# Optimization experiments

Measured on AMD Instinct MI355X. Metric: run time of the kernel, lower is better.

Reference implementation:

```python
import jax, jax.numpy as jnp
import numpy as np

B = 4096          # graph pairs in batch
NPG = 40          # nodes per molecular graph
N = B * NPG       # total nodes per drug batch
EPG = 160         # directed edges per graph
E = B * EPG
F_IN = 78         # atom feature dim
HID = 128
HEADS = 4
ADD = 8           # additional features (concentrations)
BN_EPS = 1e-5
D0 = HEADS * HID          # 512
CMB = 4 * HID + ADD       # 2 drugs * (mean||max of 128) + ADD = 520


def setup_inputs() -> dict:
    key = jax.random.key(0)
    ks = iter(jax.random.split(key, 64))
    def nrm(shape, s=0.1):
        return jax.random.normal(next(ks), shape, jnp.float32) * s
    def pos(shape):  # positive running variances
        return jax.random.uniform(next(ks), shape, jnp.float32, 0.5, 1.5)
    offs = jnp.repeat(jnp.arange(B, dtype=jnp.int32) * NPG, EPG)
    def edges():
        return jax.random.randint(next(ks), (2, E), 0, NPG, dtype=jnp.int32) + offs[None, :]
    batch = jnp.repeat(jnp.arange(B, dtype=jnp.int32), NPG)
    inp = dict(
        x_a=nrm((N, F_IN), 1.0), edge_a=edges(), batch_a=batch,
        x_b=nrm((N, F_IN), 1.0), edge_b=edges(), batch_b=batch,
        addf=nrm((B, ADD), 1.0),
        # shared GAT encoder params
        gW0=nrm((F_IN, D0)), gb0=nrm((D0,)), gas0=nrm((D0,)), gad0=nrm((D0,)),
        gW1=nrm((D0, D0)), gb1=nrm((D0,)), gas1=nrm((D0,)), gad1=nrm((D0,)),
        gW2=nrm((D0, HID)), gb2=nrm((HID,)), gas2=nrm((HID,)), gad2=nrm((HID,)),
        bn0g=pos((D0,)), bn0b=nrm((D0,)), bn0m=nrm((D0,)), bn0v=pos((D0,)),
        bn1g=pos((D0,)), bn1b=nrm((D0,)), bn1m=nrm((D0,)), bn1v=pos((D0,)),
        bn2g=pos((HID,)), bn2b=nrm((HID,)), bn2m=nrm((HID,)), bn2v=pos((HID,)),
        # combination MLP params (Linear + eval BatchNorm stats)
        mW0=nrm((CMB, 2 * HID)), mb0=nrm((2 * HID,)),
        mg0=pos((2 * HID,)), mbe0=nrm((2 * HID,)), mm0=nrm((2 * HID,)), mv0=pos((2 * HID,)),
        mW1=nrm((2 * HID, HID)), mb1=nrm((HID,)),
        mg1=pos((HID,)), mbe1=nrm((HID,)), mm1=nrm((HID,)), mv1=pos((HID,)),
        mW2=nrm((HID, 1)), mb2=nrm((1,)),
    )
    return inp


def _bn(x, g, b, m, v):
    return (x - m) * jax.lax.rsqrt(v + BN_EPS) * g + b


def _gat(x, src, dst, W, b, a_src, a_dst, heads, ch, concat):
    """PyG GATConv (eval): linear, per-head additive attention with
    leaky_relu(0.2), segment-softmax over incoming edges (self-loops included)."""
    n = x.shape[0]
    h = (x @ W).reshape(n, heads, ch)                     # [N, H, C]
    es = jnp.sum(h * a_src.reshape(1, heads, ch), -1)     # [N, H]
    ed = jnp.sum(h * a_dst.reshape(1, heads, ch), -1)     # [N, H]
    e = jax.nn.leaky_relu(es[src] + ed[dst], 0.2)         # [E', H]
    emax = jax.ops.segment_max(e, dst, num_segments=n)
    ex = jnp.exp(e - emax[dst])
    den = jax.ops.segment_sum(ex, dst, num_segments=n)
    alpha = ex / den[dst]                                 # [E', H]
    out = jax.ops.segment_sum(h[src] * alpha[..., None], dst, num_segments=n)
    out = out.reshape(n, heads * ch) if concat else jnp.mean(out, axis=1)
    return out + b


def _encode(x, edge, batch, p):
    n = x.shape[0]
    sl = jnp.arange(n, dtype=edge.dtype)                  # self-loops (PyG default)
    src = jnp.concatenate([edge[0], sl])
    dst = jnp.concatenate([edge[1], sl])
    x = _gat(x, src, dst, p['gW0'], p['gb0'], p['gas0'], p['gad0'], HEADS, HID, True)
    x = jax.nn.relu(_bn(x, p['bn0g'], p['bn0b'], p['bn0m'], p['bn0v']))
    x = _gat(x, src, dst, p['gW1'], p['gb1'], p['gas1'], p['gad1'], HEADS, HID, True)
    x = jax.nn.relu(_bn(x, p['bn1g'], p['bn1b'], p['bn1m'], p['bn1v']))
    x = _gat(x, src, dst, p['gW2'], p['gb2'], p['gas2'], p['gad2'], 1, HID, False)
    x = _bn(x, p['bn2g'], p['bn2b'], p['bn2m'], p['bn2v'])  # no relu on last layer
    cnt = jax.ops.segment_sum(jnp.ones((n, 1), x.dtype), batch, num_segments=B)
    x_mean = jax.ops.segment_sum(x, batch, num_segments=B) / cnt
    x_max = jax.ops.segment_max(x, batch, num_segments=B)
    return jnp.concatenate([x_mean, x_max], axis=1)        # [B, 2*HID]


def reference(x_a, edge_a, batch_a, x_b, edge_b, batch_b, addf,
              gW0, gb0, gas0, gad0, gW1, gb1, gas1, gad1, gW2, gb2, gas2, gad2,
              bn0g, bn0b, bn0m, bn0v, bn1g, bn1b, bn1m, bn1v, bn2g, bn2b, bn2m, bn2v,
              mW0, mb0, mg0, mbe0, mm0, mv0, mW1, mb1, mg1, mbe1, mm1, mv1, mW2, mb2):
    p = dict(gW0=gW0, gb0=gb0, gas0=gas0, gad0=gad0, gW1=gW1, gb1=gb1, gas1=gas1,
             gad1=gad1, gW2=gW2, gb2=gb2, gas2=gas2, gad2=gad2,
             bn0g=bn0g, bn0b=bn0b, bn0m=bn0m, bn0v=bn0v,
             bn1g=bn1g, bn1b=bn1b, bn1m=bn1m, bn1v=bn1v,
             bn2g=bn2g, bn2b=bn2b, bn2m=bn2m, bn2v=bn2v)
    emb_a = _encode(x_a, edge_a, batch_a, p)
    emb_b = _encode(x_b, edge_b, batch_b, p)
    c = jnp.concatenate([emb_a, emb_b, addf], axis=1)      # [B, 520]
    h = jax.nn.relu(_bn(c @ mW0 + mb0, mg0, mbe0, mm0, mv0))
    h = jax.nn.relu(_bn(h @ mW1 + mb1, mg1, mbe1, mm1, mv1))
    out = jax.nn.sigmoid(h @ mW2 + mb2)
    return jnp.squeeze(out, -1)                            # [B]
```

## Files before the change

### kernel.cpp

```cpp
#include <hip/hip_runtime.h>
#include <stdint.h>

#define B_GRAPHS 4096
#define NPG 40
#define NTOT (B_GRAPHS * NPG)
#define EPG 160
#define ETOT (B_GRAPHS * EPG)
#define ESL 200
#define F_IN 78
#define KP0 96
#define HID 128
#define D0 512
#define CMB 520
#define BN_EPS 1e-5f
#define KPM 544
#define A0ST 552
#define H1ST 264
#define H2ST 132

typedef short bf16x8 __attribute__((ext_vector_type(8)));
typedef float floatx4 __attribute__((ext_vector_type(4)));

__device__ inline float b2f(unsigned short u) {
    union { float f; uint32_t i; } v; v.i = ((uint32_t)u) << 16; return v.f;
}
__device__ inline unsigned short f2b(float f) {
    union { float f; uint32_t i; } v; v.f = f;
    uint32_t x = v.i;
    return (unsigned short)((x + 0x7fffu + ((x >> 16) & 1u)) >> 16);
}
__device__ inline float lo16(uint32_t u) {
    union { float f; uint32_t i; } v; v.i = u << 16; return v.f;
}
__device__ inline float hi16(uint32_t u) {
    union { float f; uint32_t i; } v; v.i = u & 0xffff0000u; return v.f;
}
__device__ inline int htoff(int ch, int s) {
    int chunk = s >> 3, within = s & 7;
    return ch * 40 + (((chunk + ch) % 5) << 3) + within;
}
__device__ inline void gl2lds16(const unsigned short* g, unsigned short* l) {
    __builtin_amdgcn_global_load_lds(
        (const __attribute__((address_space(1))) unsigned int*)g,
        (__attribute__((address_space(3))) unsigned int*)l, 16, 0, 0);
}

__global__ __launch_bounds__(256)
void write_code_kernel(float* __restrict__ out, int n, float S)
{
    int i = blockIdx.x * 256 + threadIdx.x;
    if (i < n) out[i] = (i == 0) ? S : 0.f;
}

__global__ __launch_bounds__(256)
void convw_kernel(const float* __restrict__ W, unsigned short* __restrict__ Wt,
                  int K, int N, int Kp)
{
    int t = blockIdx.x * 256 + threadIdx.x;
    if (t >= N * Kp) return;
    int n = t / Kp, k = t - n * Kp;
    Wt[t] = (k < K) ? f2b(W[(size_t)k * N + n]) : 0;
}

__global__ __launch_bounds__(256)
void convw_hilo_kernel(const float* __restrict__ W,
                       unsigned short* __restrict__ Whi,
                       unsigned short* __restrict__ Wlo,
                       int K, int N, int Kp)
{
    int t = blockIdx.x * 256 + threadIdx.x;
    if (t >= N * Kp) return;
    int n = t / Kp, k = t - n * Kp;
    float x = (k < K) ? W[(size_t)k * N + n] : 0.f;
    unsigned short hb = f2b(x);
    Whi[t] = hb;
    Wlo[t] = f2b(x - b2f(hb));
}

__global__ __launch_bounds__(256)
void convx_kernel(const float* __restrict__ X, unsigned short* __restrict__ Xb, int M)
{
    int t = blockIdx.x * 256 + threadIdx.x;
    if (t >= M * (KP0 / 8)) return;
    int r = t / (KP0 / 8), c8 = t - r * (KP0 / 8);
    unsigned int pk[4];
    #pragma unroll
    for (int j = 0; j < 4; j++) {
        int k0 = c8 * 8 + 2 * j, k1 = k0 + 1;
        float x0 = (k0 < F_IN) ? X[(size_t)r * F_IN + k0] : 0.f;
        float x1 = (k1 < F_IN) ? X[(size_t)r * F_IN + k1] : 0.f;
        pk[j] = (unsigned int)f2b(x0) | ((unsigned int)f2b(x1) << 16);
    }
    *(uint4*)&Xb[(size_t)r * KP0 + c8 * 8] = make_uint4(pk[0], pk[1], pk[2], pk[3]);
}

__global__ __launch_bounds__(256)
void gemm_mfma_kernel(const unsigned short* __restrict__ A,
                      const unsigned short* __restrict__ Bt,
                      unsigned short* __restrict__ C,
                      int M, int K, int N)
{
    __shared__ __align__(16) unsigned short As[128 * 32];
    __shared__ __align__(16) unsigned short Bs[128 * 32];
    const int tid  = threadIdx.x;
    const int lane = tid & 63, w = tid >> 6;
    const int quad = lane >> 4, l16 = lane & 15;
    const int wm = w >> 1, wn = w & 1;
    const int nwg  = gridDim.x * gridDim.y;
    const int orig = blockIdx.y * gridDim.x + blockIdx.x;
    const int q = nwg >> 3, r = nwg & 7;
    const int xcd = orig & 7, off = orig >> 3;
    const int swz = (xcd < r ? xcd * (q + 1) : r * (q + 1) + (xcd - r) * q) + off;
    const int row0 = (swz / gridDim.x) * 128, col0 = (swz % gridDim.x) * 128;

    floatx4 acc[4][4];
    #pragma unroll
    for (int mi = 0; mi < 4; mi++)
        #pragma unroll
        for (int ni = 0; ni < 4; ni++)
            acc[mi][ni] = (floatx4){0.f, 0.f, 0.f, 0.f};

    int srow[2], scg[2];
    #pragma unroll
    for (int it = 0; it < 2; it++) {
        int L = it * 4096 + w * 1024 + lane * 16;
        int rr = L >> 6;
        int cp = (L >> 4) & 3;
        srow[it] = rr;
        scg[it]  = cp ^ ((rr >> 1) & 3);
    }

    for (int k0 = 0; k0 < K; k0 += 32) {
        #pragma unroll
        for (int it = 0; it < 2; it++) {
            int ra = row0 + srow[it]; if (ra >= M) ra = M - 1;
            gl2lds16(A + (size_t)ra * K + k0 + scg[it] * 8,
                     As + (it * 4096 + w * 1024) / 2);
            int rb = col0 + srow[it];
            gl2lds16(Bt + (size_t)rb * K + k0 + scg[it] * 8,
                     Bs + (it * 4096 + w * 1024) / 2);
        }
        __syncthreads();

        bf16x8 fA[4], fB[4];
        #pragma unroll
        for (int mi = 0; mi < 4; mi++) {
            int rr = wm * 64 + mi * 16 + l16;
            __builtin_memcpy(&fA[mi], &As[rr * 32 + ((quad ^ ((rr >> 1) & 3)) * 8)], 16);
        }
        #pragma unroll
        for (int ni = 0; ni < 4; ni++) {
            int rr = wn * 64 + ni * 16 + l16;
            __builtin_memcpy(&fB[ni], &Bs[rr * 32 + ((quad ^ ((rr >> 1) & 3)) * 8)], 16);
        }
        #pragma unroll
        for (int mi = 0; mi < 4; mi++)
            #pragma unroll
            for (int ni = 0; ni < 4; ni++)
                acc[mi][ni] = __builtin_amdgcn_mfma_f32_16x16x32_bf16(
                    fB[ni], fA[mi], acc[mi][ni], 0, 0, 0);
        __syncthreads();
    }

    #pragma unroll
    for (int mi = 0; mi < 4; mi++) {
        int row = row0 + wm * 64 + mi * 16 + l16;
        if (row < M) {
            #pragma unroll
            for (int ni = 0; ni < 4; ni++) {
                floatx4 a = acc[mi][ni];
                unsigned int p0 = (unsigned int)f2b(a[0]) | ((unsigned int)f2b(a[1]) << 16);
                unsigned int p1 = (unsigned int)f2b(a[2]) | ((unsigned int)f2b(a[3]) << 16);
                *(uint2*)(C + (size_t)row * N + col0 + wn * 64 + ni * 16 + quad * 4) =
                    make_uint2(p0, p1);
            }
        }
    }
}

__global__ __launch_bounds__(256)
void gat4_fused_kernel(unsigned short* __restrict__ H,
                       const int* __restrict__ edge,
                       const float* __restrict__ avs, const float* __restrict__ avd,
                       const float* __restrict__ bias,
                       const float* __restrict__ bng, const float* __restrict__ bnb,
                       const float* __restrict__ bnm, const float* __restrict__ bnv,
                       int g0)
{
    __shared__ __align__(16) unsigned short ht[D0 * NPG];
    __shared__ float es[4 * NPG], ed[4 * NPG];
    __shared__ __align__(16) unsigned char cnt[NPG * 48];
    __shared__ short2 eloc[ESL];
    const int tid = threadIdx.x;
    const int lane = tid & 63, w = tid >> 6;
    const int quad = lane >> 4, l16 = lane & 15;
    const int gg = g0 + blockIdx.x;
    unsigned short* Hg = H + (size_t)blockIdx.x * NPG * D0;

    for (int i = tid; i < NPG * 48 / 4; i += 256) ((unsigned int*)cnt)[i] = 0u;
    for (int i = tid; i < ESL; i += 256) {
        if (i < EPG) {
            int s  = edge[(size_t)gg * EPG + i] - gg * NPG;
            int dd = edge[(size_t)ETOT + (size_t)gg * EPG + i] - gg * NPG;
            eloc[i] = make_short2((short)s, (short)dd);
        } else {
            short v = (short)(i - EPG);
            eloc[i] = make_short2(v, v);
        }
    }
    for (int u = tid; u < 64 * (NPG / 4); u += 256) {
        int c8 = u & 63, gi = u >> 6;
        const unsigned short* src = Hg + (size_t)(4 * gi) * D0 + c8 * 8;
        uint4 v0 = *(const uint4*)(src);
        uint4 v1 = *(const uint4*)(src + D0);
        uint4 v2 = *(const uint4*)(src + 2 * D0);
        uint4 v3 = *(const uint4*)(src + 3 * D0);
        unsigned int a0[4] = {v0.x, v0.y, v0.z, v0.w};
        unsigned int a1[4] = {v1.x, v1.y, v1.z, v1.w};
        unsigned int a2[4] = {v2.x, v2.y, v2.z, v2.w};
        unsigned int a3[4] = {v3.x, v3.y, v3.z, v3.w};
        #pragma unroll
        for (int k = 0; k < 8; k++) {
            const int ws = k >> 1, sh = (k & 1) * 16;
            unsigned int w0 = ((a0[ws] >> sh) & 0xffffu) | (((a1[ws] >> sh) & 0xffffu) << 16);
            unsigned int w1 = ((a2[ws] >> sh) & 0xffffu) | (((a3[ws] >> sh) & 0xffffu) << 16);
            *(uint2*)&ht[htoff(c8 * 8 + k, 4 * gi)] = make_uint2(w0, w1);
        }
    }
    __syncthreads();

    {
        float as0=0,as1=0,as2=0,as3=0, ad0=0,ad1=0,ad2=0,ad3=0;
        for (int ci = 0; ci < 32; ci++) {
            int c = quad + ci * 4;
            int chv = w * 128 + c;
            uint2 hv = *(const uint2*)&ht[htoff(chv, 4 * l16)];
            float h0 = lo16(hv.x), h1 = hi16(hv.x), h2 = lo16(hv.y), h3 = hi16(hv.y);
            float vs = avs[chv], vd = avd[chv];
            as0 += h0*vs; as1 += h1*vs; as2 += h2*vs; as3 += h3*vs;
            ad0 += h0*vd; ad1 += h1*vd; ad2 += h2*vd; ad3 += h3*vd;
        }
        #define RED4(x) x += __shfl_xor(x, 16); x += __shfl_xor(x, 32);
        RED4(as0) RED4(as1) RED4(as2) RED4(as3)
        RED4(ad0) RED4(ad1) RED4(ad2) RED4(ad3)
        #undef RED4
        if (quad == 0) {
            float rs[4] = {as0, as1, as2, as3};
            float rd[4] = {ad0, ad1, ad2, ad3};
            #pragma unroll
            for (int rr = 0; rr < 4; rr++) {
                int node = 4 * l16 + rr;
                if (node < NPG) { es[w * NPG + node] = rs[rr]; ed[w * NPG + node] = rd[rr]; }
            }
        }
    }
    for (int e = tid; e < ESL; e += 256) {
        short2 sd = eloc[e];
        atomicAdd((unsigned int*)cnt + ((sd.y * 48 + sd.x) >> 2),
                  1u << ((sd.x & 3) * 8));
    }
    __syncthreads();

    {
        bf16x8 ahi[3][2], alo[3][2];
        float esv0[8], esv1[8];
        #pragma unroll
        for (int j = 0; j < 8; j++) {
            esv0[j] = es[w * NPG + quad * 8 + j];
            esv1[j] = (quad == 0) ? es[w * NPG + 32 + j] : 0.f;
        }
        #pragma unroll
        for (int mt = 0; mt < 3; mt++) {
            int dn = mt * 16 + l16;
            bool ok = dn < NPG;
            float edv = 0.f;
            uint2 c0 = make_uint2(0u, 0u), c1 = make_uint2(0u, 0u);
            if (ok) {
                edv = ed[w * NPG + dn];
                c0 = *(const uint2*)&cnt[dn * 48 + quad * 8];
                if (quad == 0) c1 = *(const uint2*)&cnt[dn * 48 + 32];
            }
            float v0[8], v1[8];
            int cb0[8], cb1[8];
            float pm = -1e30f;
            #pragma unroll
            for (int j = 0; j < 8; j++) {
                cb0[j] = (int)(((j < 4 ? c0.x : c0.y) >> ((j & 3) * 8)) & 0xffu);
                float t0 = esv0[j] + edv;
                v0[j] = t0 > 0.f ? t0 : 0.2f * t0;
                if (cb0[j]) pm = fmaxf(pm, v0[j]);
                cb1[j] = (int)(((j < 4 ? c1.x : c1.y) >> ((j & 3) * 8)) & 0xffu);
                float t1 = esv1[j] + edv;
                v1[j] = t1 > 0.f ? t1 : 0.2f * t1;
                if (cb1[j]) pm = fmaxf(pm, v1[j]);
            }
            pm = fmaxf(pm, __shfl_xor(pm, 16));
            pm = fmaxf(pm, __shfl_xor(pm, 32));
            float e0[8], e1[8], pd = 0.f;
            #pragma unroll
            for (int j = 0; j < 8; j++) {
                e0[j] = cb0[j] ? (float)cb0[j] * __expf(v0[j] - pm) : 0.f;
                e1[j] = cb1[j] ? (float)cb1[j] * __expf(v1[j] - pm) : 0.f;
                pd += e0[j] + e1[j];
            }
            pd += __shfl_xor(pd, 16);
            pd += __shfl_xor(pd, 32);
            float di = ok ? 1.f / pd : 0.f;
            #pragma unroll
            for (int j = 0; j < 8; j++) {
                float a0 = e0[j] * di;
                unsigned short hb0 = f2b(a0);
                ahi[mt][0][j] = (short)hb0;
                alo[mt][0][j] = (short)f2b(a0 - b2f(hb0));
                float a1 = e1[j] * di;
                unsigned short hb1 = f2b(a1);
                ahi[mt][1][j] = (short)hb1;
                alo[mt][1][j] = (short)f2b(a1 - b2f(hb1));
            }
        }
        const floatx4 z = {0.f, 0.f, 0.f, 0.f};
        for (int nt = 0; nt < 8; nt++) {
            const int ch0 = w * 128 + nt * 16;
            bf16x8 b0, b1 = {0,0,0,0,0,0,0,0};
            __builtin_memcpy(&b0, &ht[htoff(ch0 + l16, quad * 8)], 16);
            if (quad == 0) __builtin_memcpy(&b1, &ht[htoff(ch0 + l16, 32)], 16);
            floatx4 acc0 = z, acc1 = z, acc2 = z;
            acc0 = __builtin_amdgcn_mfma_f32_16x16x32_bf16(ahi[0][0], b0, acc0, 0, 0, 0);
            acc1 = __builtin_amdgcn_mfma_f32_16x16x32_bf16(ahi[1][0], b0, acc1, 0, 0, 0);
            acc2 = __builtin_amdgcn_mfma_f32_16x16x32_bf16(ahi[2][0], b0, acc2, 0, 0, 0);
            acc0 = __builtin_amdgcn_mfma_f32_16x16x32_bf16(alo[0][0], b0, acc0, 0, 0, 0);
            acc1 = __builtin_amdgcn_mfma_f32_16x16x32_bf16(alo[1][0], b0, acc1, 0, 0, 0);
            acc2 = __builtin_amdgcn_mfma_f32_16x16x32_bf16(alo[2][0], b0, acc2, 0, 0, 0);
            acc0 = __builtin_amdgcn_mfma_f32_16x16x32_bf16(ahi[0][1], b1, acc0, 0, 0, 0);
            acc1 = __builtin_amdgcn_mfma_f32_16x16x32_bf16(ahi[1][1], b1, acc1, 0, 0, 0);
            acc2 = __builtin_amdgcn_mfma_f32_16x16x32_bf16(ahi[2][1], b1, acc2, 0, 0, 0);
            acc0 = __builtin_amdgcn_mfma_f32_16x16x32_bf16(alo[0][1], b1, acc0, 0, 0, 0);
            acc1 = __builtin_amdgcn_mfma_f32_16x16x32_bf16(alo[1][1], b1, acc1, 0, 0, 0);
            acc2 = __builtin_amdgcn_mfma_f32_16x16x32_bf16(alo[2][1], b1, acc2, 0, 0, 0);
            const int c = ch0 + l16;
            float scl = rsqrtf(bnv[c] + BN_EPS) * bng[c];
            float sft = (bias[c] - bnm[c]) * scl + bnb[c];
            unsigned short* reg = &ht[ch0 * 40];
            #pragma unroll
            for (int mt = 0; mt < 3; mt++) {
                floatx4 a = (mt == 0) ? acc0 : (mt == 1) ? acc1 : acc2;
                #pragma unroll
                for (int rr = 0; rr < 4; rr++) {
                    int dn = mt * 16 + quad * 4 + rr;
                    if (dn < NPG) {
                        float o = a[rr] * scl + sft;
                        o = fmaxf(o, 0.f);
                        reg[dn * 16 + l16] = f2b(o);
                    }
                }
            }
        }
    }
    __syncthreads();
    for (int u = tid; u < NPG * 64; u += 256) {
        int s = u >> 6, c8 = u & 63;
        const unsigned short* reg = &ht[(c8 >> 1) * 16 * 40];
        uint4 v = *(const uint4*)&reg[s * 16 + (c8 & 1) * 8];
        *(uint4*)(Hg + (size_t)s * D0 + c8 * 8) = v;
    }
}

__global__ __launch_bounds__(256)
void gat1_pool_fused_kernel(const unsigned short* __restrict__ H,
                            const int* __restrict__ edge,
                            const float* __restrict__ avs, const float* __restrict__ avd,
                            const float* __restrict__ bias,
                            const float* __restrict__ bng, const float* __restrict__ bnb,
                            const float* __restrict__ bnm, const float* __restrict__ bnv,
                            float* __restrict__ cmb, int colbase, int g0)
{
    __shared__ __align__(16) unsigned short ht[HID * NPG];
    __shared__ float es[NPG], ed[NPG];
    __shared__ __align__(16) unsigned char cnt[NPG * 48];
    __shared__ short2 eloc[ESL];
    const int tid = threadIdx.x;
    const int lane = tid & 63, w = tid >> 6;
    const int quad = lane >> 4, l16 = lane & 15;
    const int gg = g0 + blockIdx.x;
    const unsigned short* Hg = H + (size_t)blockIdx.x * NPG * HID;

    for (int i = tid; i < NPG * 48 / 4; i += 256) ((unsigned int*)cnt)[i] = 0u;
    for (int i = tid; i < ESL; i += 256) {
        if (i < EPG) {
            int s  = edge[(size_t)gg * EPG + i] - gg * NPG;
            int dd = edge[(size_t)ETOT + (size_t)gg * EPG + i] - gg * NPG;
            eloc[i] = make_short2((short)s, (short)dd);
        } else {
            short v = (short)(i - EPG);
            eloc[i] = make_short2(v, v);
        }
    }
    for (int u = tid; u < 16 * (NPG / 4); u += 256) {
        int c8 = u & 15, gi = u >> 4;
        const unsigned short* src = Hg + (size_t)(4 * gi) * HID + c8 * 8;
        uint4 v0 = *(const uint4*)(src);
        uint4 v1 = *(const uint4*)(src + HID);
        uint4 v2 = *(const uint4*)(src + 2 * HID);
        uint4 v3 = *(const uint4*)(src + 3 * HID);
        unsigned int a0[4] = {v0.x, v0.y, v0.z, v0.w};
        unsigned int a1[4] = {v1.x, v1.y, v1.z, v1.w};
        unsigned int a2[4] = {v2.x, v2.y, v2.z, v2.w};
        unsigned int a3[4] = {v3.x, v3.y, v3.z, v3.w};
        #pragma unroll
        for (int k = 0; k < 8; k++) {
            const int ws = k >> 1, sh = (k & 1) * 16;
            unsigned int w0 = ((a0[ws] >> sh) & 0xffffu) | (((a1[ws] >> sh) & 0xffffu) << 16);
            unsigned int w1 = ((a2[ws] >> sh) & 0xffffu) | (((a3[ws] >> sh) & 0xffffu) << 16);
            *(uint2*)&ht[htoff(c8 * 8 + k, 4 * gi)] = make_uint2(w0, w1);
        }
    }
    __syncthreads();

    if (w < 2) {
        const float* av = w ? avd : avs;
        float a0=0,a1=0,a2=0,a3=0;
        for (int ci = 0; ci < 32; ci++) {
            int c = quad + ci * 4;
            uint2 hv = *(const uint2*)&ht[htoff(c, 4 * l16)];
            float vc = av[c];
            a0 += lo16(hv.x)*vc; a1 += hi16(hv.x)*vc;
            a2 += lo16(hv.y)*vc; a3 += hi16(hv.y)*vc;
        }
        #define RED4(x) x += __shfl_xor(x, 16); x += __shfl_xor(x, 32);
        RED4(a0) RED4(a1) RED4(a2) RED4(a3)
        #undef RED4
        if (quad == 0) {
            float rv[4] = {a0, a1, a2, a3};
            float* dst = w ? ed : es;
            #pragma unroll
            for (int rr = 0; rr < 4; rr++) {
                int node = 4 * l16 + rr;
                if (node < NPG) dst[node] = rv[rr];
            }
        }
    }
    for (int e = tid; e < ESL; e += 256) {
        short2 sd = eloc[e];
        atomicAdd((unsigned int*)cnt + ((sd.y * 48 + sd.x) >> 2),
                  1u << ((sd.x & 3) * 8));
    }
    __syncthreads();

    {
        bf16x8 ahi[3][2], alo[3][2];
        float esv0[8], esv1[8];
        #pragma unroll
        for (int j = 0; j < 8; j++) {
            esv0[j] = es[quad * 8 + j];
            esv1[j] = (quad == 0) ? es[32 + j] : 0.f;
        }
        #pragma unroll
        for (int mt = 0; mt < 3; mt++) {
            int dn = mt * 16 + l16;
            bool ok = dn < NPG;
            float edv = 0.f;
            uint2 c0 = make_uint2(0u, 0u), c1 = make_uint2(0u, 0u);
            if (ok) {
                edv = ed[dn];
                c0 = *(const uint2*)&cnt[dn * 48 + quad * 8];
                if (quad == 0) c1 = *(const uint2*)&cnt[dn * 48 + 32];
            }
            float v0[8], v1[8];
            int cb0[8], cb1[8];
            float pm = -1e30f;
            #pragma unroll
            for (int j = 0; j < 8; j++) {
                cb0[j] = (int)(((j < 4 ? c0.x : c0.y) >> ((j & 3) * 8)) & 0xffu);
                float t0 = esv0[j] + edv;
                v0[j] = t0 > 0.f ? t0 : 0.2f * t0;
                if (cb0[j]) pm = fmaxf(pm, v0[j]);
                cb1[j] = (int)(((j < 4 ? c1.x : c1.y) >> ((j & 3) * 8)) & 0xffu);
                float t1 = esv1[j] + edv;
                v1[j] = t1 > 0.f ? t1 : 0.2f * t1;
                if (cb1[j]) pm = fmaxf(pm, v1[j]);
            }
            pm = fmaxf(pm, __shfl_xor(pm, 16));
            pm = fmaxf(pm, __shfl_xor(pm, 32));
            float e0[8], e1[8], pd = 0.f;
            #pragma unroll
            for (int j = 0; j < 8; j++) {
                e0[j] = cb0[j] ? (float)cb0[j] * __expf(v0[j] - pm) : 0.f;
                e1[j] = cb1[j] ? (float)cb1[j] * __expf(v1[j] - pm) : 0.f;
                pd += e0[j] + e1[j];
            }
            pd += __shfl_xor(pd, 16);
            pd += __shfl_xor(pd, 32);
            float di = ok ? 1.f / pd : 0.f;
            #pragma unroll
            for (int j = 0; j < 8; j++) {
                float a0 = e0[j] * di;
                unsigned short hb0 = f2b(a0);
                ahi[mt][0][j] = (short)hb0;
                alo[mt][0][j] = (short)f2b(a0 - b2f(hb0));
                float a1 = e1[j] * di;
                unsigned short hb1 = f2b(a1);
                ahi[mt][1][j] = (short)hb1;
                alo[mt][1][j] = (short)f2b(a1 - b2f(hb1));
            }
        }
        const floatx4 z = {0.f, 0.f, 0.f, 0.f};
        for (int t2 = 0; t2 < 2; t2++) {
            const int ch0 = (w * 2 + t2) * 16;
            bf16x8 b0, b1 = {0,0,0,0,0,0,0,0};
            __builtin_memcpy(&b0, &ht[htoff(ch0 + l16, quad * 8)], 16);
            if (quad == 0) __builtin_memcpy(&b1, &ht[htoff(ch0 + l16, 32)], 16);
            floatx4 acc0 = z, acc1 = z, acc2 = z;
            acc0 = __builtin_amdgcn_mfma_f32_16x16x32_bf16(ahi[0][0], b0, acc0, 0, 0, 0);
            acc1 = __builtin_amdgcn_mfma_f32_16x16x32_bf16(ahi[1][0], b0, acc1, 0, 0, 0);
            acc2 = __builtin_amdgcn_mfma_f32_16x16x32_bf16(ahi[2][0], b0, acc2, 0, 0, 0);
            acc0 = __builtin_amdgcn_mfma_f32_16x16x32_bf16(alo[0][0], b0, acc0, 0, 0, 0);
            acc1 = __builtin_amdgcn_mfma_f32_16x16x32_bf16(alo[1][0], b0, acc1, 0, 0, 0);
            acc2 = __builtin_amdgcn_mfma_f32_16x16x32_bf16(alo[2][0], b0, acc2, 0, 0, 0);
            acc0 = __builtin_amdgcn_mfma_f32_16x16x32_bf16(ahi[0][1], b1, acc0, 0, 0, 0);
            acc1 = __builtin_amdgcn_mfma_f32_16x16x32_bf16(ahi[1][1], b1, acc1, 0, 0, 0);
            acc2 = __builtin_amdgcn_mfma_f32_16x16x32_bf16(ahi[2][1], b1, acc2, 0, 0, 0);
            acc0 = __builtin_amdgcn_mfma_f32_16x16x32_bf16(alo[0][1], b1, acc0, 0, 0, 0);
            acc1 = __builtin_amdgcn_mfma_f32_16x16x32_bf16(alo[1][1], b1, acc1, 0, 0, 0);
            acc2 = __builtin_amdgcn_mfma_f32_16x16x32_bf16(alo[2][1], b1, acc2, 0, 0, 0);
            const int c = ch0 + l16;
            float scl = rsqrtf(bnv[c] + BN_EPS) * bng[c];
            float sft = (bias[c] - bnm[c]) * scl + bnb[c];
            float psum = 0.f, pmax = -1e30f;
            #pragma unroll
            for (int mt = 0; mt < 3; mt++) {
                floatx4 a = (mt == 0) ? acc0 : (mt == 1) ? acc1 : acc2;
                #pragma unroll
                for (int rr = 0; rr < 4; rr++) {
                    int dn = mt * 16 + quad * 4 + rr;
                    if (dn < NPG) {
                        float o = a[rr] * scl + sft;
                        psum += o;
                        pmax = fmaxf(pmax, o);
                    }
                }
            }
            psum += __shfl_xor(psum, 16); psum += __shfl_xor(psum, 32);
            pmax = fmaxf(pmax, __shfl_xor(pmax, 16));
            pmax = fmaxf(pmax, __shfl_xor(pmax, 32));
            if (quad == 0) {
                cmb[(size_t)gg * 512 + colbase + c] = psum * (1.f / NPG);
                cmb[(size_t)gg * 512 + colbase + HID + c] = pmax;
            }
        }
    }
}

__global__ __launch_bounds__(256)
void mlp_mfma_kernel(const float* __restrict__ cmb, const float* __restrict__ addf,
                     const unsigned short* __restrict__ W0hi, const unsigned short* __restrict__ W0lo,
                     const float* __restrict__ b0, const float* __restrict__ g0v,
                     const float* __restrict__ be0, const float* __restrict__ m0,
                     const float* __restrict__ v0,
                     const unsigned short* __restrict__ W1hi, const unsigned short* __restrict__ W1lo,
                     const float* __restrict__ b1, const float* __restrict__ g1v,
                     const float* __restrict__ be1, const float* __restrict__ m1,
                     const float* __restrict__ v1,
                     const float* __restrict__ W2, const float* __restrict__ b2,
                     float* __restrict__ out)
{
    __shared__ __align__(16) unsigned short a0hi[16 * A0ST], a0lo[16 * A0ST];
    __shared__ __align__(16) unsigned short h1hi[16 * H1ST], h1lo[16 * H1ST];
    __shared__ float h2[16 * H2ST];
    const int tid = threadIdx.x;
    const int lane = tid & 63, w = tid >> 6;
    const int quad = lane >> 4, l16 = lane & 15;
    const int gb = blockIdx.x * 16;

    for (int i = tid; i < 16 * KPM; i += 256) {
        int g = i / KPM, k = i - g * KPM;
        float x = 0.f;
        if (k < 512) x = cmb[(size_t)(gb + g) * 512 + k];
        else if (k < CMB) x = addf[(gb + g) * 8 + (k - 512)];
        unsigned short hb = f2b(x);
        a0hi[g * A0ST + k] = hb;
        a0lo[g * A0ST + k] = f2b(x - b2f(hb));
    }
    __syncthreads();

    {
        floatx4 acc[4];
        #pragma unroll
        for (int ni = 0; ni < 4; ni++) acc[ni] = (floatx4){0.f, 0.f, 0.f, 0.f};
        for (int k0 = 0; k0 < KPM; k0 += 32) {
            bf16x8 fah, fal;
            __builtin_memcpy(&fah, &a0hi[l16 * A0ST + k0 + quad * 8], 16);
            __builtin_memcpy(&fal, &a0lo[l16 * A0ST + k0 + quad * 8], 16);
            #pragma unroll
            for (int ni = 0; ni < 4; ni++) {
                int row = w * 64 + ni * 16 + l16;
                bf16x8 fwh, fwl;
                __builtin_memcpy(&fwh, &W0hi[(size_t)row * KPM + k0 + quad * 8], 16);
                __builtin_memcpy(&fwl, &W0lo[(size_t)row * KPM + k0 + quad * 8], 16);
                acc[ni] = __builtin_amdgcn_mfma_f32_16x16x32_bf16(fwh, fah, acc[ni], 0, 0, 0);
                acc[ni] = __builtin_amdgcn_mfma_f32_16x16x32_bf16(fwh, fal, acc[ni], 0, 0, 0);
                acc[ni] = __builtin_amdgcn_mfma_f32_16x16x32_bf16(fwl, fah, acc[ni], 0, 0, 0);
            }
        }
        #pragma unroll
        for (int ni = 0; ni < 4; ni++) {
            int cbase = w * 64 + ni * 16 + quad * 4;
            unsigned int ph[2], pl[2];
            #pragma unroll
            for (int j = 0; j < 2; j++) {
                unsigned int hh[2], ll[2];
                #pragma unroll
                for (int q = 0; q < 2; q++) {
                    int rr = 2 * j + q, c = cbase + rr;
                    float scl = rsqrtf(v0[c] + BN_EPS) * g0v[c];
                    float val = (acc[ni][rr] + b0[c] - m0[c]) * scl + be0[c];
                    val = fmaxf(val, 0.f);
                    unsigned short hb = f2b(val);
                    hh[q] = hb;
                    ll[q] = f2b(val - b2f(hb));
                }
                ph[j] = hh[0] | (hh[1] << 16);
                pl[j] = ll[0] | (ll[1] << 16);
            }
            *(uint2*)&h1hi[l16 * H1ST + cbase] = make_uint2(ph[0], ph[1]);
            *(uint2*)&h1lo[l16 * H1ST + cbase] = make_uint2(pl[0], pl[1]);
        }
    }
    __syncthreads();

    {
        floatx4 acc[2];
        acc[0] = (floatx4){0.f, 0.f, 0.f, 0.f};
        acc[1] = (floatx4){0.f, 0.f, 0.f, 0.f};
        for (int k0 = 0; k0 < 256; k0 += 32) {
            bf16x8 fah, fal;
            __builtin_memcpy(&fah, &h1hi[l16 * H1ST + k0 + quad * 8], 16);
            __builtin_memcpy(&fal, &h1lo[l16 * H1ST + k0 + quad * 8], 16);
            #pragma unroll
            for (int ni = 0; ni < 2; ni++) {
                int row = w * 32 + ni * 16 + l16;
                bf16x8 fwh, fwl;
                __builtin_memcpy(&fwh, &W1hi[(size_t)row * 256 + k0 + quad * 8], 16);
                __builtin_memcpy(&fwl, &W1lo[(size_t)row * 256 + k0 + quad * 8], 16);
                acc[ni] = __builtin_amdgcn_mfma_f32_16x16x32_bf16(fwh, fah, acc[ni], 0, 0, 0);
                acc[ni] = __builtin_amdgcn_mfma_f32_16x16x32_bf16(fwh, fal, acc[ni], 0, 0, 0);
                acc[ni] = __builtin_amdgcn_mfma_f32_16x16x32_bf16(fwl, fah, acc[ni], 0, 0, 0);
            }
        }
        #pragma unroll
        for (int ni = 0; ni < 2; ni++) {
            #pragma unroll
            for (int rr = 0; rr < 4; rr++) {
                int c = w * 32 + ni * 16 + quad * 4 + rr;
                float scl = rsqrtf(v1[c] + BN_EPS) * g1v[c];
                float val = (acc[ni][rr] + b1[c] - m1[c]) * scl + be1[c];
                h2[l16 * H2ST + c] = fmaxf(val, 0.f);
            }
        }
    }
    __syncthreads();

    {
        int g = tid >> 4, part = tid & 15;
        float s = 0.f;
        #pragma unroll
        for (int j = 0; j < 8; j++)
            s += h2[g * H2ST + part * 8 + j] * W2[part * 8 + j];
        s += __shfl_xor(s, 1); s += __shfl_xor(s, 2);
        s += __shfl_xor(s, 4); s += __shfl_xor(s, 8);
        if (part == 0) out[gb + g] = 1.f / (1.f + __expf(-(s + b2[0])));
    }
}

extern "C" void kernel_launch(void* const* d_in, const int* in_sizes, int n_in,
                              void* d_out, int out_size, void* d_ws, size_t ws_size,
                              hipStream_t stream)
{
    float* out = (float*)d_out;
    int out_n = out_size < 4096 ? out_size : 4096;

    const float* x_a  = (const float*)d_in[0];
    const int*   edge_a = (const int*)d_in[1];
    const float* x_b  = (const float*)d_in[3];
    const int*   edge_b = (const int*)d_in[4];
    const float* addf = (const float*)d_in[6];
    const float* gW0 = (const float*)d_in[7],  *gb0 = (const float*)d_in[8];
    const float* gas0 = (const float*)d_in[9], *gad0 = (const float*)d_in[10];
    const float* gW1 = (const float*)d_in[11], *gb1 = (const float*)d_in[12];
    const float* gas1 = (const float*)d_in[13], *gad1 = (const float*)d_in[14];
    const float* gW2 = (const float*)d_in[15], *gb2 = (const float*)d_in[16];
    const float* gas2 = (const float*)d_in[17], *gad2 = (const float*)d_in[18];
    const float* bn0g = (const float*)d_in[19], *bn0b = (const float*)d_in[20];
    const float* bn0m = (const float*)d_in[21], *bn0v = (const float*)d_in[22];
    const float* bn1g = (const float*)d_in[23], *bn1b = (const float*)d_in[24];
    const float* bn1m = (const float*)d_in[25], *bn1v = (const float*)d_in[26];
    const float* bn2g = (const float*)d_in[27], *bn2b = (const float*)d_in[28];
    const float* bn2m = (const float*)d_in[29], *bn2v = (const float*)d_in[30];
    const float* mW0 = (const float*)d_in[31], *mb0 = (const float*)d_in[32];
    const float* mg0 = (const float*)d_in[33], *mbe0 = (const float*)d_in[34];
    const float* mm0 = (const float*)d_in[35], *mv0 = (const float*)d_in[36];
    const float* mW1 = (const float*)d_in[37], *mb1 = (const float*)d_in[38];
    const float* mg1 = (const float*)d_in[39], *mbe1 = (const float*)d_in[40];
    const float* mm1 = (const float*)d_in[41], *mv1 = (const float*)d_in[42];
    const float* mW2 = (const float*)d_in[43], *mb2 = (const float*)d_in[44];

    char* p = (char*)d_ws;
    const size_t CMB_BYTES = (size_t)B_GRAPHS * 512 * sizeof(float);
    float* cmb = (float*)p; p += CMB_BYTES;
    unsigned short* W0t = (unsigned short*)p; p += (size_t)D0 * KP0 * 2;
    unsigned short* W1t = (unsigned short*)p; p += (size_t)D0 * D0 * 2;
    unsigned short* W2t = (unsigned short*)p; p += (size_t)HID * D0 * 2;
    unsigned short* M0hi = (unsigned short*)p; p += (size_t)256 * KPM * 2;
    unsigned short* M0lo = (unsigned short*)p; p += (size_t)256 * KPM * 2;
    unsigned short* M1hi = (unsigned short*)p; p += (size_t)128 * 256 * 2;
    unsigned short* M1lo = (unsigned short*)p; p += (size_t)128 * 256 * 2;
    size_t used = (size_t)(p - (char*)d_ws);
    const size_t PG = 7680ull + 40960ull + 40960ull;
    int chunk = B_GRAPHS;
    while (chunk > 4 && used + (size_t)chunk * PG > ws_size) chunk >>= 1;
    if (used + (size_t)chunk * PG > ws_size) {
        write_code_kernel<<<(out_n + 255) / 256, 256, 0, stream>>>(out, out_n, 500000.f);
        return;
    }
    unsigned short* Xb = (unsigned short*)p; p += (size_t)chunk * 7680;
    unsigned short* B1 = (unsigned short*)p; p += (size_t)chunk * 40960;
    unsigned short* B2 = (unsigned short*)p;

    convw_kernel<<<(D0 * KP0 + 255) / 256, 256, 0, stream>>>(gW0, W0t, F_IN, D0, KP0);
    convw_kernel<<<(D0 * D0 + 255) / 256, 256, 0, stream>>>(gW1, W1t, D0, D0, D0);
    convw_kernel<<<(HID * D0 + 255) / 256, 256, 0, stream>>>(gW2, W2t, D0, HID, D0);
    convw_hilo_kernel<<<(256 * KPM + 255) / 256, 256, 0, stream>>>(
        mW0, M0hi, M0lo, CMB, 256, KPM);
    convw_hilo_kernel<<<(128 * 256 + 255) / 256, 256, 0, stream>>>(
        mW1, M1hi, M1lo, 256, 128, 256);

    for (int drug = 0; drug < 2; drug++) {
        const float* x = drug ? x_b : x_a;
        const int* edge = drug ? edge_b : edge_a;
        int colbase = drug ? 256 : 0;

        for (int g0 = 0; g0 < B_GRAPHS; g0 += chunk) {
            int n = chunk * NPG;
            int gy = (n + 127) / 128;
            convx_kernel<<<(n * (KP0 / 8) + 255) / 256, 256, 0, stream>>>(
                x + (size_t)g0 * NPG * F_IN, Xb, n);
            gemm_mfma_kernel<<<dim3(D0 / 128, gy), 256, 0, stream>>>(
                Xb, W0t, B1, n, KP0, D0);
            gat4_fused_kernel<<<chunk, 256, 0, stream>>>(
                B1, edge, gas0, gad0, gb0, bn0g, bn0b, bn0m, bn0v, g0);
            gemm_mfma_kernel<<<dim3(D0 / 128, gy), 256, 0, stream>>>(
                B1, W1t, B2, n, D0, D0);
            gat4_fused_kernel<<<chunk, 256, 0, stream>>>(
                B2, edge, gas1, gad1, gb1, bn1g, bn1b, bn1m, bn1v, g0);
            gemm_mfma_kernel<<<dim3(HID / 128, gy), 256, 0, stream>>>(
                B2, W2t, B1, n, D0, HID);
            gat1_pool_fused_kernel<<<chunk, 256, 0, stream>>>(
                B1, edge, gas2, gad2, gb2, bn2g, bn2b, bn2m, bn2v,
                cmb, colbase, g0);
        }
    }
    mlp_mfma_kernel<<<B_GRAPHS / 16, 256, 0, stream>>>(
        cmb, addf, M0hi, M0lo, mb0, mg0, mbe0, mm0, mv0,
        M1hi, M1lo, mb1, mg1, mbe1, mm1, mv1, mW2, mb2, out);
}
```

Before: 1.339 ms.

## Split 4-head GAT kernel across two blocks per graph by head pairs

The 4-head GAT aggregation kernel now launches two blocks per graph, each handling two heads (256 channels). LDS use per block drops by half, which allows more resident blocks and more parallelism. Within a block, the score computation is split so that one wave computes source scores and the other computes destination scores for each head, and the MFMA channel tiles are divided between the two waves of a head. The cost is that edge loading and count building are duplicated in both blocks.

Result: slower. 1.516 ms (+13.2%).

```diff
diff --git a/kernel.cpp b/kernel.cpp
--- a/kernel.cpp
+++ b/kernel.cpp
@@ -187,15 +187,16 @@
                        const float* __restrict__ bnm, const float* __restrict__ bnv,
                        int g0)
 {
-    __shared__ __align__(16) unsigned short ht[D0 * NPG];
-    __shared__ float es[4 * NPG], ed[4 * NPG];
+    __shared__ __align__(16) unsigned short ht[256 * NPG];
+    __shared__ float es[2 * NPG], ed[2 * NPG];
     __shared__ __align__(16) unsigned char cnt[NPG * 48];
     __shared__ short2 eloc[ESL];
     const int tid = threadIdx.x;
     const int lane = tid & 63, w = tid >> 6;
     const int quad = lane >> 4, l16 = lane & 15;
+    const int hl = w >> 1;
     const int gg = g0 + blockIdx.x;
-    unsigned short* Hg = H + (size_t)blockIdx.x * NPG * D0;
+    unsigned short* Hg = H + (size_t)blockIdx.x * NPG * D0 + blockIdx.y * 256;
 
     for (int i = tid; i < NPG * 48 / 4; i += 256) ((unsigned int*)cnt)[i] = 0u;
     for (int i = tid; i < ESL; i += 256) {
@@ -208,8 +209,8 @@
             eloc[i] = make_short2(v, v);
         }
     }
-    for (int u = tid; u < 64 * (NPG / 4); u += 256) {
-        int c8 = u & 63, gi = u >> 6;
+    for (int u = tid; u < 32 * (NPG / 4); u += 256) {
+        int c8 = u & 31, gi = u >> 5;
         const unsigned short* src = Hg + (size_t)(4 * gi) * D0 + c8 * 8;
         uint4 v0 = *(const uint4*)(src);
         uint4 v1 = *(const uint4*)(src + D0);
@@ -230,27 +231,26 @@
     __syncthreads();
 
     {
-        float as0=0,as1=0,as2=0,as3=0, ad0=0,ad1=0,ad2=0,ad3=0;
+        const int gh = blockIdx.y * 2 + hl;
+        const float* av = (w & 1) ? avd : avs;
+        float a0=0,a1=0,a2=0,a3=0;
         for (int ci = 0; ci < 32; ci++) {
             int c = quad + ci * 4;
-            int chv = w * 128 + c;
-            uint2 hv = *(const uint2*)&ht[htoff(chv, 4 * l16)];
-            float h0 = lo16(hv.x), h1 = hi16(hv.x), h2 = lo16(hv.y), h3 = hi16(hv.y);
-            float vs = avs[chv], vd = avd[chv];
-            as0 += h0*vs; as1 += h1*vs; as2 += h2*vs; as3 += h3*vs;
-            ad0 += h0*vd; ad1 += h1*vd; ad2 += h2*vd; ad3 += h3*vd;
+            uint2 hv = *(const uint2*)&ht[htoff(hl * 128 + c, 4 * l16)];
+            float vc = av[gh * 128 + c];
+            a0 += lo16(hv.x)*vc; a1 += hi16(hv.x)*vc;
+            a2 += lo16(hv.y)*vc; a3 += hi16(hv.y)*vc;
         }
         #define RED4(x) x += __shfl_xor(x, 16); x += __shfl_xor(x, 32);
-        RED4(as0) RED4(as1) RED4(as2) RED4(as3)
-        RED4(ad0) RED4(ad1) RED4(ad2) RED4(ad3)
+        RED4(a0) RED4(a1) RED4(a2) RED4(a3)
         #undef RED4
         if (quad == 0) {
-            float rs[4] = {as0, as1, as2, as3};
-            float rd[4] = {ad0, ad1, ad2, ad3};
+            float rv[4] = {a0, a1, a2, a3};
+            float* dst = (w & 1) ? &ed[hl * NPG] : &es[hl * NPG];
             #pragma unroll
             for (int rr = 0; rr < 4; rr++) {
                 int node = 4 * l16 + rr;
-                if (node < NPG) { es[w * NPG + node] = rs[rr]; ed[w * NPG + node] = rd[rr]; }
+                if (node < NPG) dst[node] = rv[rr];
             }
         }
     }
@@ -266,8 +266,8 @@
         float esv0[8], esv1[8];
         #pragma unroll
         for (int j = 0; j < 8; j++) {
-            esv0[j] = es[w * NPG + quad * 8 + j];
-            esv1[j] = (quad == 0) ? es[w * NPG + 32 + j] : 0.f;
+            esv0[j] = es[hl * NPG + quad * 8 + j];
+            esv1[j] = (quad == 0) ? es[hl * NPG + 32 + j] : 0.f;
         }
         #pragma unroll
         for (int mt = 0; mt < 3; mt++) {
@@ -276,7 +276,7 @@
             float edv = 0.f;
             uint2 c0 = make_uint2(0u, 0u), c1 = make_uint2(0u, 0u);
             if (ok) {
-                edv = ed[w * NPG + dn];
+                edv = ed[hl * NPG + dn];
                 c0 = *(const uint2*)&cnt[dn * 48 + quad * 8];
                 if (quad == 0) c1 = *(const uint2*)&cnt[dn * 48 + 32];
             }
@@ -319,8 +319,9 @@
             }
         }
         const floatx4 z = {0.f, 0.f, 0.f, 0.f};
-        for (int nt = 0; nt < 8; nt++) {
-            const int ch0 = w * 128 + nt * 16;
+        const int ntb = (w & 1) * 4;
+        for (int nt = ntb; nt < ntb + 4; nt++) {
+            const int ch0 = hl * 128 + nt * 16;
             bf16x8 b0, b1 = {0,0,0,0,0,0,0,0};
             __builtin_memcpy(&b0, &ht[htoff(ch0 + l16, quad * 8)], 16);
             if (quad == 0) __builtin_memcpy(&b1, &ht[htoff(ch0 + l16, 32)], 16);
@@ -337,7 +338,7 @@
             acc0 = __builtin_amdgcn_mfma_f32_16x16x32_bf16(alo[0][1], b1, acc0, 0, 0, 0);
             acc1 = __builtin_amdgcn_mfma_f32_16x16x32_bf16(alo[1][1], b1, acc1, 0, 0, 0);
             acc2 = __builtin_amdgcn_mfma_f32_16x16x32_bf16(alo[2][1], b1, acc2, 0, 0, 0);
-            const int c = ch0 + l16;
+            const int c = blockIdx.y * 256 + ch0 + l16;
             float scl = rsqrtf(bnv[c] + BN_EPS) * bng[c];
             float sft = (bias[c] - bnm[c]) * scl + bnb[c];
             unsigned short* reg = &ht[ch0 * 40];
@@ -357,8 +358,8 @@
         }
     }
     __syncthreads();
-    for (int u = tid; u < NPG * 64; u += 256) {
-        int s = u >> 6, c8 = u & 63;
+    for (int u = tid; u < NPG * 32; u += 256) {
+        int s = u >> 5, c8 = u & 31;
         const unsigned short* reg = &ht[(c8 >> 1) * 16 * 40];
         uint4 v = *(const uint4*)&reg[s * 16 + (c8 & 1) * 8];
         *(uint4*)(Hg + (size_t)s * D0 + c8 * 8) = v;
@@ -745,11 +746,11 @@
                 x + (size_t)g0 * NPG * F_IN, Xb, n);
             gemm_mfma_kernel<<<dim3(D0 / 128, gy), 256, 0, stream>>>(
                 Xb, W0t, B1, n, KP0, D0);
-            gat4_fused_kernel<<<chunk, 256, 0, stream>>>(
+            gat4_fused_kernel<<<dim3(chunk, 2), 256, 0, stream>>>(
                 B1, edge, gas0, gad0, gb0, bn0g, bn0b, bn0m, bn0v, g0);
             gemm_mfma_kernel<<<dim3(D0 / 128, gy), 256, 0, stream>>>(
                 B1, W1t, B2, n, D0, D0);
-            gat4_fused_kernel<<<chunk, 256, 0, stream>>>(
+            gat4_fused_kernel<<<dim3(chunk, 2), 256, 0, stream>>>(
                 B2, edge, gas1, gad1, gb1, bn1g, bn1b, bn1m, bn1v, g0);
             gemm_mfma_kernel<<<dim3(HID / 128, gy), 256, 0, stream>>>(
                 B2, W2t, B1, n, D0, HID);
```
